# Performance work log

Hardware: AMD Instinct MI355X
Metric: run time of the kernel (lower is better)

Reference implementation:

```python
import jax, jax.numpy as jnp
import numpy as np

EPS = 1e-5
GROUPS = 8


def setup_inputs() -> dict:
    key = jax.random.key(0)
    ks = jax.random.split(key, 6)
    C = 512
    B, H, W = 4, 64, 64
    s = 1.0 / np.sqrt(C)
    return {
        "x": jax.random.normal(ks[0], (B, C, H, W), dtype=jnp.float32),
        "gn_gamma": jnp.ones((C,), jnp.float32),
        "gn_beta": jnp.zeros((C,), jnp.float32),
        "wq": jax.random.normal(ks[1], (C, C), jnp.float32) * s,
        "bq": jnp.zeros((C,), jnp.float32),
        "wk": jax.random.normal(ks[2], (C, C), jnp.float32) * s,
        "bk": jnp.zeros((C,), jnp.float32),
        "wv": jax.random.normal(ks[3], (C, C), jnp.float32) * s,
        "bv": jnp.zeros((C,), jnp.float32),
        "wp": jax.random.normal(ks[4], (C, C), jnp.float32) * s,
        "bp": jnp.zeros((C,), jnp.float32),
    }


def _group_norm(x, gamma, beta):
    b, c, h, w = x.shape
    xg = x.reshape(b, GROUPS, c // GROUPS, h, w)
    mu = xg.mean(axis=(2, 3, 4), keepdims=True)
    var = xg.var(axis=(2, 3, 4), keepdims=True)
    xn = ((xg - mu) * jax.lax.rsqrt(var + EPS)).reshape(b, c, h, w)
    return xn * gamma[None, :, None, None] + beta[None, :, None, None]


def _conv1x1(x, w, b):
    # 1x1 conv == channel-mixing matmul: [O,C] x [B,C,H,W] -> [B,O,H,W]
    return jnp.einsum('oc,bchw->bohw', w, x) + b[None, :, None, None]


def reference(x, gn_gamma, gn_beta, wq, bq, wk, bk, wv, bv, wp, bp):
    b, c, h, w = x.shape
    xn = _group_norm(x, gn_gamma, gn_beta)  # note: residual uses normalized x, as in source
    q = _conv1x1(xn, wq, bq).reshape(b, c, h * w)
    k = _conv1x1(xn, wk, bk).reshape(b, c, h * w)
    v = _conv1x1(xn, wv, bv).reshape(b, c, h * w)
    scale = jnp.asarray(c, x.dtype) ** 0.5
    attn = jnp.einsum('bci,bcj->bij', q, k) / scale  # [b, hw, hw]
    attn = jax.nn.softmax(attn, axis=2)
    out = jnp.einsum('bij,bcj->bci', attn, v).reshape(b, c, h, w)
    out = _conv1x1(out, wp, bp)
    return xn + out
```

## Files before the change

### kernel.cpp

```cpp
#include <hip/hip_runtime.h>
#include <hip/hip_bf16.h>


typedef unsigned short u16;
typedef unsigned char u8;
typedef __bf16 bf16x8 __attribute__((ext_vector_type(8)));
typedef float f32x4 __attribute__((ext_vector_type(4)));
typedef float f32x16 __attribute__((ext_vector_type(16)));
typedef int i32x4 __attribute__((ext_vector_type(4)));
typedef int i32x8 __attribute__((ext_vector_type(8)));
typedef unsigned short u16x4 __attribute__((ext_vector_type(4)));

#define CDIM 512
#define NPOS 4096
#define NBATCH 4

__device__ __forceinline__ u16 f2bf(float x) {
  union { float f; unsigned u; } c; c.f = x;
  unsigned u = c.u;
  u += 0x7fffu + ((u >> 16) & 1u);
  return (u16)(u >> 16);
}
__device__ __forceinline__ float bf2f(u16 h) {
  union { unsigned u; float f; } c; c.u = ((unsigned)h) << 16;
  return c.f;
}
__device__ __forceinline__ unsigned pk4_fp8(float a, float b, float c, float d) {
  unsigned v = __builtin_amdgcn_cvt_pk_fp8_f32(a, b, 0, false);
  v = __builtin_amdgcn_cvt_pk_fp8_f32(c, d, v, true);
  return v;
}

__device__ __forceinline__ void async16(const u16* g, u16* l) {
  __builtin_amdgcn_global_load_lds(
      (const __attribute__((address_space(1))) unsigned int*)g,
      (__attribute__((address_space(3))) unsigned int*)l, 16, 0, 0);
}
__device__ __forceinline__ void async16b(const u8* g, u8* l) {
  __builtin_amdgcn_global_load_lds(
      (const __attribute__((address_space(1))) unsigned int*)g,
      (__attribute__((address_space(3))) unsigned int*)l, 16, 0, 0);
}

__device__ __forceinline__ void drain_barrier() {
  asm volatile("s_waitcnt vmcnt(0)" ::: "memory");
  __builtin_amdgcn_s_barrier();
}

__device__ __forceinline__ float wred_sum(float v) {
#pragma unroll
  for (int o = 32; o > 0; o >>= 1) v += __shfl_xor(v, o, 64);
  return v;
}

__global__ __launch_bounds__(256) void gn_partial(const float* __restrict__ x,
                                                  float* __restrict__ stats) {
  int gidx = blockIdx.x >> 3;
  int slice = blockIdx.x & 7;
  const float4* src = (const float4*)x + (long)gidx * 65536 + (long)slice * 8192;
  float s = 0.f, ss = 0.f;
  for (int i = threadIdx.x; i < 8192; i += 256) {
    float4 v = src[i];
    s  += v.x + v.y + v.z + v.w;
    ss += v.x * v.x + v.y * v.y + v.z * v.z + v.w * v.w;
  }
  s = wred_sum(s); ss = wred_sum(ss);
  __shared__ float r1[4], r2[4];
  int lane = threadIdx.x & 63, wave = threadIdx.x >> 6;
  if (lane == 0) { r1[wave] = s; r2[wave] = ss; }
  __syncthreads();
  if (threadIdx.x == 0) {
    atomicAdd(&stats[gidx * 2 + 0], r1[0] + r1[1] + r1[2] + r1[3]);
    atomicAdd(&stats[gidx * 2 + 1], r2[0] + r2[1] + r2[2] + r2[3]);
  }
}

__global__ __launch_bounds__(256) void norm_trans(const float* __restrict__ x,
                                                  const float* __restrict__ stats,
                                                  const float* __restrict__ gamma,
                                                  const float* __restrict__ beta,
                                                  u16* __restrict__ xnb,
                                                  u16* __restrict__ xnT) {
  __shared__ float tile[32][33];
  int b = blockIdx.z, c0 = blockIdx.y * 32, p0 = blockIdx.x * 32;
  int g = (b << 3) + (c0 >> 6);
  float cnt = 1.f / 262144.f;
  float mu = stats[g * 2 + 0] * cnt;
  float ms = stats[g * 2 + 1] * cnt;
  float rstd = rsqrtf(ms - mu * mu + 1e-5f);
  int tp = threadIdx.x & 31, tc = threadIdx.x >> 5;
#pragma unroll
  for (int r = 0; r < 4; r++) {
    int cl = tc + r * 8;
    int c = c0 + cl;
    long idx = ((long)(b * CDIM + c)) * NPOS + p0 + tp;
    float v = (x[idx] - mu) * rstd * gamma[c] + beta[c];
    xnb[idx] = f2bf(v);
    tile[cl][tp] = v;
  }
  __syncthreads();
#pragma unroll
  for (int r = 0; r < 4; r++) {
    int pl = tc + r * 8, cl = tp;
    xnT[((long)(b * NPOS + p0 + pl)) * CDIM + c0 + cl] = f2bf(tile[cl][pl]);
  }
}

__global__ __launch_bounds__(256) void cvt4(const float* __restrict__ a, const float* __restrict__ b,
                                            const float* __restrict__ c, const float* __restrict__ d,
                                            u16* __restrict__ oa, u16* __restrict__ ob,
                                            u16* __restrict__ oc, u16* __restrict__ od) {
  int i = blockIdx.x * 256 + threadIdx.x;
  const float* src; u16* dst;
  switch (blockIdx.y) {
    case 0: src = a; dst = oa; break;
    case 1: src = b; dst = ob; break;
    case 2: src = c; dst = oc; break;
    default: src = d; dst = od; break;
  }
  dst[i] = f2bf(src[i]);
}

template <int MODE, int BN>
__global__ __launch_bounds__(BN * 2, 2) void gemm_bt(
    const u16* __restrict__ A, const u16* __restrict__ B,
    void* __restrict__ Cp, const float* __restrict__ bias,
    const float* __restrict__ bias1, const u16* __restrict__ residb,
    int N, int K, int lda, int ldb,
    long sA, long sB, long sC, long sR) {
  __shared__ u16 Asm[2][128 * 64];
  __shared__ u16 Bsm[2][BN * 64];
  constexpr int NT = BN * 2;
  constexpr int STEP = NT / 8;
  int bz = blockIdx.z;
  A += (long)bz * sA;
  B += (long)bz * sB;
  int bm = blockIdx.y, bn = blockIdx.x;
  int tid = threadIdx.x;
  int lane = tid & 63, wave = tid >> 6;
  int wm = (wave & 1) * 64, wn = (wave >> 1) * 64;

  int row0 = tid >> 3;
  int ko = (tid & 7) * 8;
  int kos = ko ^ ((row0 & 7) * 8);
  f32x4 acc[4][4] = {};
  int row16 = lane & 15;
  int kq = (lane >> 4) * 8;

  auto stage = [&](int buf, int k0) {
#pragma unroll
    for (int r = 0; r < 128 / STEP; r++) {
      int row = row0 + r * STEP;
      async16(A + (long)(bm * 128 + row) * lda + k0 + kos, &Asm[buf][row * 64 + ko]);
    }
#pragma unroll
    for (int r = 0; r < BN / STEP; r++) {
      int row = row0 + r * STEP;
      async16(B + (long)(bn * BN + row) * ldb + k0 + kos, &Bsm[buf][row * 64 + ko]);
    }
  };

  stage(0, 0);
  drain_barrier();
  int cur = 0;
  for (int k0 = 0; k0 < K; k0 += 64) {
    if (k0 + 64 < K) stage(cur ^ 1, k0 + 64);
#pragma unroll
    for (int s2 = 0; s2 < 2; s2++) {
      bf16x8 af[4], bfr[4];
#pragma unroll
      for (int i = 0; i < 4; i++) {
        int row = wm + i * 16 + row16;
        af[i] = *(const bf16x8*)&Asm[cur][row * 64 + ((s2 * 32 + kq) ^ ((row & 7) * 8))];
      }
#pragma unroll
      for (int j = 0; j < 4; j++) {
        int row = wn + j * 16 + row16;
        bfr[j] = *(const bf16x8*)&Bsm[cur][row * 64 + ((s2 * 32 + kq) ^ ((row & 7) * 8))];
      }
      __builtin_amdgcn_s_setprio(1);
#pragma unroll
      for (int i = 0; i < 4; i++)
#pragma unroll
        for (int j = 0; j < 4; j++)
          acc[i][j] = __builtin_amdgcn_mfma_f32_16x16x32_bf16(bfr[j], af[i], acc[i][j], 0, 0, 0);
      __builtin_amdgcn_s_setprio(0);
    }
    drain_barrier();
    cur ^= 1;
  }

  int mcol = lane & 15, rb = (lane >> 4) * 4;
  long zC = (long)bz * sC;
#pragma unroll
  for (int i = 0; i < 4; i++) {
    int gm = bm * 128 + wm + i * 16 + mcol;
    float bm_add = 0.f;
    if constexpr (MODE == 5 || MODE == 6) bm_add = bias[gm];
#pragma unroll
    for (int j = 0; j < 4; j++) {
      int gn0 = bn * BN + wn + j * 16 + rb;
      long off = zC + (long)gm * N + gn0;
      float v[4];
#pragma unroll
      for (int r = 0; r < 4; r++) v[r] = acc[i][j][r];
      if constexpr (MODE == 0) {
        const float* bb = (gn0 < 512) ? (bias + gn0) : (bias1 + (gn0 - 512));
#pragma unroll
        for (int r = 0; r < 4; r++) v[r] += bb[r];
        *(unsigned*)&((u8*)Cp)[off] = pk4_fp8(v[0], v[1], v[2], v[3]);
      }
      if constexpr (MODE == 5) {
#pragma unroll
        for (int r = 0; r < 4; r++) v[r] += bm_add;
        *(unsigned*)&((u8*)Cp)[off] = pk4_fp8(v[0], v[1], v[2], v[3]);
      }
      if constexpr (MODE == 6) {
        u16x4 rv = *(const u16x4*)&residb[(long)bz * sR + (long)gm * N + gn0];
        f32x4 o;
#pragma unroll
        for (int r = 0; r < 4; r++) o[r] = v[r] + bm_add + bf2f(rv[r]);
        *(f32x4*)&((float*)Cp)[off] = o;
      }
    }
  }
}

__global__ __launch_bounds__(512, 2) void fattn(const u8* __restrict__ QKf8,
                                                const u8* __restrict__ Vf8,
                                                u16* __restrict__ H, float scale) {
  __shared__ u8 Ksm[65536];
  __shared__ u8 Vsm[65536];
  __shared__ u8 Pp[8192];
  __shared__ float lsum[4][64];
  int tid = threadIdx.x, lane = tid & 63, w = tid >> 6;
  int l31 = lane & 31, h = lane >> 5;
  int wi = w >> 2, wj = w & 3;
  int bm = blockIdx.x, bz = blockIdx.z;
  const u8* QKb = QKf8 + (long)bz * 4194304;
  const u8* Vb  = Vf8 + (long)bz * 2097152;

  i32x8 qf[8];
  {
    const u8* qrow = QKb + (long)(bm * 64 + wi * 32 + l31) * 1024 + h * 32;
#pragma unroll
    for (int s = 0; s < 8; s++) {
      i32x4 lo = *(const i32x4*)(qrow + s * 64);
      i32x4 hi = *(const i32x4*)(qrow + s * 64 + 16);
      qf[s] = __builtin_shufflevector(lo, hi, 0, 1, 2, 3, 4, 5, 6, 7);
    }
  }

  auto stageK = [&](int t) {
#pragma unroll
    for (int r = 0; r < 8; r++) {
      int zz = tid + r * 512;
      int j = zz >> 5, pos = zz & 31;
      int gch = (pos & 24) | ((pos & 7) ^ (j & 7));
      async16b(QKb + (long)(t * 128 + j) * 1024 + 512 + gch * 16, &Ksm[zz * 16]);
    }
  };
  auto stageV = [&](int t) {
#pragma unroll
    for (int r = 0; r < 8; r++) {
      int zz = tid + r * 512;
      int c = zz >> 3, pos = zz & 7;
      int gch = pos ^ (c & 7);
      async16b(Vb + (long)c * 4096 + t * 128 + gch * 16, &Vsm[zz * 16]);
    }
  };

  f32x16 acc[2][2] = {};
  float rsum = 0.f;
  int i = wi * 32 + l31;
  int jr = wj * 32 + l31;

  stageK(0);

  for (int t = 0; t < 32; t++) {
    __syncthreads();
    stageV(t);
    f32x16 s16 = {};
#pragma unroll
    for (int s = 0; s < 8; s++) {
      int p0 = 4 * s + 2 * h;
      int pos0 = (p0 & 24) | ((p0 & 7) ^ (jr & 7));
      int pos1 = (p0 & 24) | (((p0 + 1) & 7) ^ (jr & 7));
      i32x4 lo = *(const i32x4*)&Ksm[jr * 512 + pos0 * 16];
      i32x4 hi = *(const i32x4*)&Ksm[jr * 512 + pos1 * 16];
      i32x8 bfk = __builtin_shufflevector(lo, hi, 0, 1, 2, 3, 4, 5, 6, 7);
      __builtin_amdgcn_s_setprio(1);
      s16 = __builtin_amdgcn_mfma_scale_f32_32x32x64_f8f6f4(
          bfk, qf[s], s16, 0, 0, 0, 0x7F7F7F7F, 0, 0x7F7F7F7F);
      __builtin_amdgcn_s_setprio(0);
    }
    float pv[16];
    float rs = 0.f;
#pragma unroll
    for (int r = 0; r < 16; r++) { pv[r] = __expf(s16[r] * scale); rs += pv[r]; }
    rsum += rs + __shfl_xor(rs, 32, 64);
#pragma unroll
    for (int g = 0; g < 4; g++) {
      int ch = wj * 2 + (g >> 1);
      int pos = ch ^ (i & 7);
      *(unsigned*)&Pp[i * 128 + pos * 16 + 8 * (g & 1) + 4 * h] =
          pk4_fp8(pv[4 * g], pv[4 * g + 1], pv[4 * g + 2], pv[4 * g + 3]);
    }
    __syncthreads();
    if (t < 31) stageK(t + 1);
#pragma unroll
    for (int kk = 0; kk < 2; kk++) {
      i32x8 afp[2], bfv[2];
#pragma unroll
      for (int mr = 0; mr < 2; mr++) {
        int ii = mr * 32 + l31;
        int c0 = kk * 4 + h * 2;
        i32x4 lo = *(const i32x4*)&Pp[ii * 128 + ((c0) ^ (ii & 7)) * 16];
        i32x4 hi = *(const i32x4*)&Pp[ii * 128 + ((c0 + 1) ^ (ii & 7)) * 16];
        afp[mr] = __builtin_shufflevector(lo, hi, 0, 1, 2, 3, 4, 5, 6, 7);
      }
#pragma unroll
      for (int nr = 0; nr < 2; nr++) {
        int c = w * 64 + nr * 32 + l31;
        int g0 = kk * 4 + h * 2;
        i32x4 lo = *(const i32x4*)&Vsm[c * 128 + ((g0) ^ (c & 7)) * 16];
        i32x4 hi = *(const i32x4*)&Vsm[c * 128 + ((g0 + 1) ^ (c & 7)) * 16];
        bfv[nr] = __builtin_shufflevector(lo, hi, 0, 1, 2, 3, 4, 5, 6, 7);
      }
      __builtin_amdgcn_s_setprio(1);
#pragma unroll
      for (int mr = 0; mr < 2; mr++)
#pragma unroll
        for (int nr = 0; nr < 2; nr++)
          acc[mr][nr] = __builtin_amdgcn_mfma_scale_f32_32x32x64_f8f6f4(
              bfv[nr], afp[mr], acc[mr][nr], 0, 0, 0, 0x7F7F7F7F, 0, 0x7F7F7F7F);
      __builtin_amdgcn_s_setprio(0);
    }
  }

  if (lane < 32) lsum[wj][wi * 32 + l31] = rsum;
  __syncthreads();
#pragma unroll
  for (int mr = 0; mr < 2; mr++) {
    int li = mr * 32 + l31;
    float lt = lsum[0][li] + lsum[1][li] + lsum[2][li] + lsum[3][li];
    float inv = 1.f / lt;
    long hrow = ((long)bz * NPOS + bm * 64 + li) * 512;
#pragma unroll
    for (int nr = 0; nr < 2; nr++) {
#pragma unroll
      for (int g = 0; g < 4; g++) {
        u16x4 o;
#pragma unroll
        for (int r = 0; r < 4; r++) o[r] = f2bf(acc[mr][nr][4 * g + r] * inv);
        *(u16x4*)&H[hrow + w * 64 + nr * 32 + 8 * g + 4 * h] = o;
      }
    }
  }
}

extern "C" void kernel_launch(void* const* d_in, const int* in_sizes, int n_in,
                              void* d_out, int out_size, void* d_ws, size_t ws_size,
                              hipStream_t stream) {
  const float* x     = (const float*)d_in[0];
  const float* gamma = (const float*)d_in[1];
  const float* beta  = (const float*)d_in[2];
  const float* wq = (const float*)d_in[3];
  const float* bq = (const float*)d_in[4];
  const float* wk = (const float*)d_in[5];
  const float* bk = (const float*)d_in[6];
  const float* wv = (const float*)d_in[7];
  const float* bv = (const float*)d_in[8];
  const float* wp = (const float*)d_in[9];
  const float* bp = (const float*)d_in[10];
  float* out = (float*)d_out;

  char* W = (char*)d_ws;
  float* stats = (float*)(W + 0);
  u16* xnb  = (u16*)(W + 65792);
  u16* xnT  = (u16*)(W + 16843008);
  u16* wqkb = (u16*)(W + 33620224);
  u16* wvb  = (u16*)(W + 34668800);
  u16* wpb  = (u16*)(W + 35193088);
  u8*  QKf8 = (u8*)(W + 37290240);
  u8*  Vf8  = (u8*)(W + 54067456);
  u16* Hws  = (u16*)(W + 62456064);
  (void)in_sizes; (void)n_in; (void)out_size; (void)ws_size;

  hipMemsetAsync(W, 0, 256, stream);
  gn_partial<<<256, 256, 0, stream>>>(x, stats);
  norm_trans<<<dim3(128, 16, 4), 256, 0, stream>>>(x, stats, gamma, beta, xnb, xnT);
  cvt4<<<dim3(1024, 4), 256, 0, stream>>>(wq, wk, wv, wp, wqkb, wqkb + 262144, wvb, wpb);

  const long NC = (long)NPOS * CDIM;
  const long CN = (long)CDIM * NPOS;
  const float scale = 0.044194173824159216f;

  gemm_bt<0, 128><<<dim3(8, 128, 1), 256, 0, stream>>>(xnT, wqkb, QKf8, bq, bk, nullptr,
      1024, CDIM, CDIM, CDIM, 0, 0, 0, 0);
  gemm_bt<5, 128><<<dim3(32, 4, 4), 256, 0, stream>>>(wvb, xnT, Vf8, bv, nullptr, nullptr,
      NPOS, CDIM, CDIM, CDIM, 0, NC, CN, 0);
  fattn<<<dim3(64, 1, NBATCH), 512, 0, stream>>>(QKf8, Vf8, Hws, scale);
  gemm_bt<6, 128><<<dim3(32, 4, 4), 256, 0, stream>>>(wpb, Hws, (void*)out, bp, nullptr, xnb,
      NPOS, CDIM, CDIM, CDIM, 0, (long)NPOS * CDIM, CN, CN);
}
```

Baseline: 282.6 us.

## Halve attention key tile to 64 and use 4-wave blocks with wider V accumulators

The flash-attention kernel now runs with 256 threads (4 waves) instead of 512, and processes 64 keys per iteration over 64 iterations instead of 128 keys over 32. Each wave owns 128 output channels with a 2x4 accumulator array, and the K, V and P shared-memory tiles are halved and re-swizzled, so the P tile is reused across more MFMAs per load. The exponential is switched to exp2f with the log2(e) factor folded into the scale. This cuts LDS use per block, which may allow more resident blocks, but doubles the barrier count and raises accumulator register pressure.

```diff
diff --git a/kernel.cpp b/kernel.cpp
--- a/kernel.cpp
+++ b/kernel.cpp
@@ -226,16 +226,16 @@
   }
 }
 
-__global__ __launch_bounds__(512, 2) void fattn(const u8* __restrict__ QKf8,
+__global__ __launch_bounds__(256, 2) void fattn(const u8* __restrict__ QKf8,
                                                 const u8* __restrict__ Vf8,
-                                                u16* __restrict__ H, float scale) {
-  __shared__ u8 Ksm[65536];
-  __shared__ u8 Vsm[65536];
-  __shared__ u8 Pp[8192];
-  __shared__ float lsum[4][64];
+                                                u16* __restrict__ H, float scale2) {
+  __shared__ u8 Ksm[32768];
+  __shared__ u8 Vsm[32768];
+  __shared__ u8 Pp[4096];
+  __shared__ float lsum[2][64];
   int tid = threadIdx.x, lane = tid & 63, w = tid >> 6;
   int l31 = lane & 31, h = lane >> 5;
-  int wi = w >> 2, wj = w & 3;
+  int wi = w >> 1, wj = w & 1;
   int bm = blockIdx.x, bz = blockIdx.z;
   const u8* QKb = QKf8 + (long)bz * 4194304;
   const u8* Vb  = Vf8 + (long)bz * 2097152;
@@ -254,30 +254,34 @@
   auto stageK = [&](int t) {
 #pragma unroll
     for (int r = 0; r < 8; r++) {
-      int zz = tid + r * 512;
+      int zz = tid + r * 256;
       int j = zz >> 5, pos = zz & 31;
       int gch = (pos & 24) | ((pos & 7) ^ (j & 7));
-      async16b(QKb + (long)(t * 128 + j) * 1024 + 512 + gch * 16, &Ksm[zz * 16]);
+      async16b(QKb + (long)(t * 64 + j) * 1024 + 512 + gch * 16, &Ksm[zz * 16]);
     }
   };
   auto stageV = [&](int t) {
 #pragma unroll
     for (int r = 0; r < 8; r++) {
-      int zz = tid + r * 512;
-      int c = zz >> 3, pos = zz & 7;
-      int gch = pos ^ (c & 7);
-      async16b(Vb + (long)c * 4096 + t * 128 + gch * 16, &Vsm[zz * 16]);
+      int zz = tid + r * 256;
+      int ldsrow = zz >> 3;
+      int gch = (zz & 7) ^ (ldsrow & 7);
+      int c = ldsrow * 2 + (gch >> 2);
+      int c16 = gch & 3;
+      async16b(Vb + (long)c * 4096 + t * 64 + c16 * 16, &Vsm[zz * 16]);
     }
   };
 
-  f32x16 acc[2][2] = {};
+  f32x16 acc[2][4] = {};
   float rsum = 0.f;
   int i = wi * 32 + l31;
   int jr = wj * 32 + l31;
+  int ilr = i >> 1, isw = ilr & 7;
+  int pgw = (i & 1) * 4;
 
   stageK(0);
 
-  for (int t = 0; t < 32; t++) {
+  for (int t = 0; t < 64; t++) {
     __syncthreads();
     stageV(t);
     f32x16 s16 = {};
@@ -297,43 +301,40 @@
     float pv[16];
     float rs = 0.f;
 #pragma unroll
-    for (int r = 0; r < 16; r++) { pv[r] = __expf(s16[r] * scale); rs += pv[r]; }
+    for (int r = 0; r < 16; r++) { pv[r] = exp2f(s16[r] * scale2); rs += pv[r]; }
     rsum += rs + __shfl_xor(rs, 32, 64);
 #pragma unroll
     for (int g = 0; g < 4; g++) {
-      int ch = wj * 2 + (g >> 1);
-      int pos = ch ^ (i & 7);
-      *(unsigned*)&Pp[i * 128 + pos * 16 + 8 * (g & 1) + 4 * h] =
+      int jc = wj * 2 + (g >> 1);
+      int chunk = (pgw + jc) ^ isw;
+      *(unsigned*)&Pp[ilr * 128 + chunk * 16 + (g & 1) * 8 + 4 * h] =
           pk4_fp8(pv[4 * g], pv[4 * g + 1], pv[4 * g + 2], pv[4 * g + 3]);
     }
     __syncthreads();
-    if (t < 31) stageK(t + 1);
-#pragma unroll
-    for (int kk = 0; kk < 2; kk++) {
-      i32x8 afp[2], bfv[2];
-#pragma unroll
-      for (int mr = 0; mr < 2; mr++) {
-        int ii = mr * 32 + l31;
-        int c0 = kk * 4 + h * 2;
-        i32x4 lo = *(const i32x4*)&Pp[ii * 128 + ((c0) ^ (ii & 7)) * 16];
-        i32x4 hi = *(const i32x4*)&Pp[ii * 128 + ((c0 + 1) ^ (ii & 7)) * 16];
-        afp[mr] = __builtin_shufflevector(lo, hi, 0, 1, 2, 3, 4, 5, 6, 7);
-      }
-#pragma unroll
-      for (int nr = 0; nr < 2; nr++) {
-        int c = w * 64 + nr * 32 + l31;
-        int g0 = kk * 4 + h * 2;
-        i32x4 lo = *(const i32x4*)&Vsm[c * 128 + ((g0) ^ (c & 7)) * 16];
-        i32x4 hi = *(const i32x4*)&Vsm[c * 128 + ((g0 + 1) ^ (c & 7)) * 16];
-        bfv[nr] = __builtin_shufflevector(lo, hi, 0, 1, 2, 3, 4, 5, 6, 7);
-      }
+    if (t < 63) stageK(t + 1);
+    i32x8 afp[2];
+#pragma unroll
+    for (int mr = 0; mr < 2; mr++) {
+      int ii = mr * 32 + l31;
+      int lr = ii >> 1, sw = lr & 7;
+      int g0 = (ii & 1) * 4 + h * 2;
+      i32x4 lo = *(const i32x4*)&Pp[lr * 128 + ((g0) ^ sw) * 16];
+      i32x4 hi = *(const i32x4*)&Pp[lr * 128 + ((g0 + 1) ^ sw) * 16];
+      afp[mr] = __builtin_shufflevector(lo, hi, 0, 1, 2, 3, 4, 5, 6, 7);
+    }
+#pragma unroll
+    for (int nr = 0; nr < 4; nr++) {
+      int c = w * 128 + nr * 32 + l31;
+      int lr = c >> 1, sw = lr & 7;
+      int g0 = (c & 1) * 4 + h * 2;
+      i32x4 lo = *(const i32x4*)&Vsm[lr * 128 + ((g0) ^ sw) * 16];
+      i32x4 hi = *(const i32x4*)&Vsm[lr * 128 + ((g0 + 1) ^ sw) * 16];
+      i32x8 bfv = __builtin_shufflevector(lo, hi, 0, 1, 2, 3, 4, 5, 6, 7);
       __builtin_amdgcn_s_setprio(1);
 #pragma unroll
       for (int mr = 0; mr < 2; mr++)
-#pragma unroll
-        for (int nr = 0; nr < 2; nr++)
-          acc[mr][nr] = __builtin_amdgcn_mfma_scale_f32_32x32x64_f8f6f4(
-              bfv[nr], afp[mr], acc[mr][nr], 0, 0, 0, 0x7F7F7F7F, 0, 0x7F7F7F7F);
+        acc[mr][nr] = __builtin_amdgcn_mfma_scale_f32_32x32x64_f8f6f4(
+            bfv, afp[mr], acc[mr][nr], 0, 0, 0, 0x7F7F7F7F, 0, 0x7F7F7F7F);
       __builtin_amdgcn_s_setprio(0);
     }
   }
@@ -343,17 +344,17 @@
 #pragma unroll
   for (int mr = 0; mr < 2; mr++) {
     int li = mr * 32 + l31;
-    float lt = lsum[0][li] + lsum[1][li] + lsum[2][li] + lsum[3][li];
+    float lt = lsum[0][li] + lsum[1][li];
     float inv = 1.f / lt;
     long hrow = ((long)bz * NPOS + bm * 64 + li) * 512;
 #pragma unroll
-    for (int nr = 0; nr < 2; nr++) {
+    for (int nr = 0; nr < 4; nr++) {
 #pragma unroll
       for (int g = 0; g < 4; g++) {
         u16x4 o;
 #pragma unroll
         for (int r = 0; r < 4; r++) o[r] = f2bf(acc[mr][nr][4 * g + r] * inv);
-        *(u16x4*)&H[hrow + w * 64 + nr * 32 + 8 * g + 4 * h] = o;
+        *(u16x4*)&H[hrow + w * 128 + nr * 32 + 8 * g + 4 * h] = o;
       }
     }
   }
@@ -395,12 +396,13 @@
   const long NC = (long)NPOS * CDIM;
   const long CN = (long)CDIM * NPOS;
   const float scale = 0.044194173824159216f;
+  const float scale2 = scale * 1.4426950408889634f;
 
   gemm_bt<0, 128><<<dim3(8, 128, 1), 256, 0, stream>>>(xnT, wqkb, QKf8, bq, bk, nullptr,
       1024, CDIM, CDIM, CDIM, 0, 0, 0, 0);
   gemm_bt<5, 128><<<dim3(32, 4, 4), 256, 0, stream>>>(wvb, xnT, Vf8, bv, nullptr, nullptr,
       NPOS, CDIM, CDIM, CDIM, 0, NC, CN, 0);
-  fattn<<<dim3(64, 1, NBATCH), 512, 0, stream>>>(QKf8, Vf8, Hws, scale);
+  fattn<<<dim3(64, 1, NBATCH), 256, 0, stream>>>(QKf8, Vf8, Hws, scale2);
   gemm_bt<6, 128><<<dim3(32, 4, 4), 256, 0, stream>>>(wpb, Hws, (void*)out, bp, nullptr, xnb,
       NPOS, CDIM, CDIM, CDIM, 0, (long)NPOS * CDIM, CN, CN);
 }
```

Measured after the change: 382.2 us. 1.35x slower.

## Software-pipeline fattn so PV of the previous tile overlaps the next QK tile

Applied to the files above, without the earlier changes.

Restructures the attention loop so the P·V MMA for tile t-1 runs after the QK scores for tile t, using a double-buffered P tile. V loads are issued only after the V fragments are read into registers. The change also swaps __expf for exp2f with a prescaled log2e factor, remaps block IDs so each XCD handles one batch, transposes the P layout in LDS, and relaxes launch bounds to one block per CU. The aim is to hide barrier and LDS latency between the two MMA phases and improve L2 locality. In exchange it adds register pressure from holding bfv across phases and uses more LDS.

```diff
diff --git a/kernel.cpp b/kernel.cpp
--- a/kernel.cpp
+++ b/kernel.cpp
@@ -44,6 +44,14 @@
 
 __device__ __forceinline__ void drain_barrier() {
   asm volatile("s_waitcnt vmcnt(0)" ::: "memory");
+  __builtin_amdgcn_s_barrier();
+}
+__device__ __forceinline__ void vm_barrier() {
+  asm volatile("s_waitcnt vmcnt(0)" ::: "memory");
+  __builtin_amdgcn_s_barrier();
+}
+__device__ __forceinline__ void lgkm_barrier() {
+  asm volatile("s_waitcnt lgkmcnt(0)" ::: "memory");
   __builtin_amdgcn_s_barrier();
 }
 
@@ -226,17 +234,20 @@
   }
 }
 
-__global__ __launch_bounds__(512, 2) void fattn(const u8* __restrict__ QKf8,
+__global__ __launch_bounds__(512, 1) void fattn(const u8* __restrict__ QKf8,
                                                 const u8* __restrict__ Vf8,
-                                                u16* __restrict__ H, float scale) {
+                                                u16* __restrict__ H, float scale2) {
   __shared__ u8 Ksm[65536];
   __shared__ u8 Vsm[65536];
-  __shared__ u8 Pp[8192];
+  __shared__ u8 Pp[2][8192];
   __shared__ float lsum[4][64];
   int tid = threadIdx.x, lane = tid & 63, w = tid >> 6;
   int l31 = lane & 31, h = lane >> 5;
   int wi = w >> 2, wj = w & 3;
-  int bm = blockIdx.x, bz = blockIdx.z;
+  int lid = blockIdx.x + 64 * blockIdx.z;
+  int xcd = lid & 7, slot = lid >> 3;
+  int bz = xcd >> 1;
+  int bm = (xcd & 1) * 32 + slot;
   const u8* QKb = QKf8 + (long)bz * 4194304;
   const u8* Vb  = Vf8 + (long)bz * 2097152;
 
@@ -278,8 +289,7 @@
   stageK(0);
 
   for (int t = 0; t < 32; t++) {
-    __syncthreads();
-    stageV(t);
+    vm_barrier();
     f32x16 s16 = {};
 #pragma unroll
     for (int s = 0; s < 8; s++) {
@@ -294,35 +304,82 @@
           bfk, qf[s], s16, 0, 0, 0, 0x7F7F7F7F, 0, 0x7F7F7F7F);
       __builtin_amdgcn_s_setprio(0);
     }
-    float pv[16];
-    float rs = 0.f;
-#pragma unroll
-    for (int r = 0; r < 16; r++) { pv[r] = __expf(s16[r] * scale); rs += pv[r]; }
-    rsum += rs + __shfl_xor(rs, 32, 64);
-#pragma unroll
-    for (int g = 0; g < 4; g++) {
-      int ch = wj * 2 + (g >> 1);
-      int pos = ch ^ (i & 7);
-      *(unsigned*)&Pp[i * 128 + pos * 16 + 8 * (g & 1) + 4 * h] =
-          pk4_fp8(pv[4 * g], pv[4 * g + 1], pv[4 * g + 2], pv[4 * g + 3]);
-    }
-    __syncthreads();
+    {
+      float pv[16];
+      float rs = 0.f;
+#pragma unroll
+      for (int r = 0; r < 16; r++) { pv[r] = exp2f(s16[r] * scale2); rs += pv[r]; }
+      rsum += rs + __shfl_xor(rs, 32, 64);
+      u8* Pw = &Pp[t & 1][0];
+#pragma unroll
+      for (int g = 0; g < 4; g++) {
+        int jc = wj * 2 + (g >> 1);
+        *(unsigned*)&Pw[jc * 1024 + i * 16 + 8 * (g & 1) + 4 * h] =
+            pk4_fp8(pv[4 * g], pv[4 * g + 1], pv[4 * g + 2], pv[4 * g + 3]);
+      }
+    }
+    lgkm_barrier();
     if (t < 31) stageK(t + 1);
+    if (t > 0) {
+      i32x8 bfv[2][2];
+#pragma unroll
+      for (int kk = 0; kk < 2; kk++) {
+        int g0 = kk * 4 + h * 2;
+#pragma unroll
+        for (int nr = 0; nr < 2; nr++) {
+          int c = w * 64 + nr * 32 + l31;
+          i32x4 lo = *(const i32x4*)&Vsm[c * 128 + ((g0) ^ (c & 7)) * 16];
+          i32x4 hi = *(const i32x4*)&Vsm[c * 128 + ((g0 + 1) ^ (c & 7)) * 16];
+          bfv[kk][nr] = __builtin_shufflevector(lo, hi, 0, 1, 2, 3, 4, 5, 6, 7);
+        }
+      }
+      lgkm_barrier();
+      stageV(t);
+      const u8* Pr = &Pp[(t ^ 1) & 1][0];
+#pragma unroll
+      for (int kk = 0; kk < 2; kk++) {
+        int kb = 4 * kk + 2 * h;
+        i32x8 afp[2];
+#pragma unroll
+        for (int mr = 0; mr < 2; mr++) {
+          int ii = mr * 32 + l31;
+          i32x4 lo = *(const i32x4*)&Pr[kb * 1024 + ii * 16];
+          i32x4 hi = *(const i32x4*)&Pr[(kb + 1) * 1024 + ii * 16];
+          afp[mr] = __builtin_shufflevector(lo, hi, 0, 1, 2, 3, 4, 5, 6, 7);
+        }
+        __builtin_amdgcn_s_setprio(1);
+#pragma unroll
+        for (int mr = 0; mr < 2; mr++)
+#pragma unroll
+          for (int nr = 0; nr < 2; nr++)
+            acc[mr][nr] = __builtin_amdgcn_mfma_scale_f32_32x32x64_f8f6f4(
+                bfv[kk][nr], afp[mr], acc[mr][nr], 0, 0, 0, 0x7F7F7F7F, 0, 0x7F7F7F7F);
+        __builtin_amdgcn_s_setprio(0);
+      }
+    } else {
+      lgkm_barrier();
+      stageV(0);
+    }
+  }
+
+  vm_barrier();
+  {
+    const u8* Pr = &Pp[1][0];
 #pragma unroll
     for (int kk = 0; kk < 2; kk++) {
+      int kb = 4 * kk + 2 * h;
+      int g0 = kk * 4 + h * 2;
       i32x8 afp[2], bfv[2];
 #pragma unroll
       for (int mr = 0; mr < 2; mr++) {
         int ii = mr * 32 + l31;
-        int c0 = kk * 4 + h * 2;
-        i32x4 lo = *(const i32x4*)&Pp[ii * 128 + ((c0) ^ (ii & 7)) * 16];
-        i32x4 hi = *(const i32x4*)&Pp[ii * 128 + ((c0 + 1) ^ (ii & 7)) * 16];
+        i32x4 lo = *(const i32x4*)&Pr[kb * 1024 + ii * 16];
+        i32x4 hi = *(const i32x4*)&Pr[(kb + 1) * 1024 + ii * 16];
         afp[mr] = __builtin_shufflevector(lo, hi, 0, 1, 2, 3, 4, 5, 6, 7);
       }
 #pragma unroll
       for (int nr = 0; nr < 2; nr++) {
         int c = w * 64 + nr * 32 + l31;
-        int g0 = kk * 4 + h * 2;
         i32x4 lo = *(const i32x4*)&Vsm[c * 128 + ((g0) ^ (c & 7)) * 16];
         i32x4 hi = *(const i32x4*)&Vsm[c * 128 + ((g0 + 1) ^ (c & 7)) * 16];
         bfv[nr] = __builtin_shufflevector(lo, hi, 0, 1, 2, 3, 4, 5, 6, 7);
@@ -395,12 +452,13 @@
   const long NC = (long)NPOS * CDIM;
   const long CN = (long)CDIM * NPOS;
   const float scale = 0.044194173824159216f;
+  const float scale2 = scale * 1.4426950408889634f;
 
   gemm_bt<0, 128><<<dim3(8, 128, 1), 256, 0, stream>>>(xnT, wqkb, QKf8, bq, bk, nullptr,
       1024, CDIM, CDIM, CDIM, 0, 0, 0, 0);
   gemm_bt<5, 128><<<dim3(32, 4, 4), 256, 0, stream>>>(wvb, xnT, Vf8, bv, nullptr, nullptr,
       NPOS, CDIM, CDIM, CDIM, 0, NC, CN, 0);
-  fattn<<<dim3(64, 1, NBATCH), 512, 0, stream>>>(QKf8, Vf8, Hws, scale);
+  fattn<<<dim3(64, 1, NBATCH), 512, 0, stream>>>(QKf8, Vf8, Hws, scale2);
   gemm_bt<6, 128><<<dim3(32, 4, 4), 256, 0, stream>>>(wpb, Hws, (void*)out, bp, nullptr, xnb,
       NPOS, CDIM, CDIM, CDIM, 0, (long)NPOS * CDIM, CN, CN);
 }
```

After: 326.3 us. 1.15x slower.
